# Optimization experiments

Measured on AMD Instinct MI355X. Metric: run time of the kernel, lower is better.

## Reference

```python
import jax, jax.numpy as jnp
import numpy as np

D_MODEL = 1024
NUM_HEADS = 16
D_HEAD = D_MODEL // NUM_HEADS
THETA = 10000.0
NEG_INF = -1e9


def apply_rope(x, theta=THETA):
    # x: (..., S, Dh) with interleaved pairs (2i, 2i+1)
    S, Dh = x.shape[-2], x.shape[-1]
    inv_freq = 1.0 / (theta ** (jnp.arange(0, Dh, 2, dtype=jnp.float32) / Dh))  # (Dh/2,)
    ang = jnp.arange(S, dtype=jnp.float32)[:, None] * inv_freq[None, :]          # (S, Dh/2)
    cos, sin = jnp.cos(ang), jnp.sin(ang)
    x1 = x[..., 0::2]
    x2 = x[..., 1::2]
    r1 = x1 * cos - x2 * sin
    r2 = x1 * sin + x2 * cos
    # interleave back
    return jnp.stack([r1, r2], axis=-1).reshape(x.shape)


def setup_inputs() -> dict:
    key = jax.random.key(0)
    ks = jax.random.split(key, 5)
    B, S = 2, 2048
    scale = 1.0 / np.sqrt(D_MODEL)
    return {
        "x": jax.random.normal(ks[0], (B, S, D_MODEL), dtype=jnp.float32),
        "Wq": jax.random.normal(ks[1], (D_MODEL, D_MODEL), dtype=jnp.float32) * scale,
        "Wk": jax.random.normal(ks[2], (D_MODEL, D_MODEL), dtype=jnp.float32) * scale,
        "Wv": jax.random.normal(ks[3], (D_MODEL, D_MODEL), dtype=jnp.float32) * scale,
        "Wo": jax.random.normal(ks[4], (D_MODEL, D_MODEL), dtype=jnp.float32) * scale,
    }


def reference(x, Wq, Wk, Wv, Wo):
    B, S, _ = x.shape
    def split_heads(t):
        return t.reshape(B, S, NUM_HEADS, D_HEAD).transpose(0, 2, 1, 3)  # (B,H,S,Dh)
    # nn.Linear(bias=False): y = x @ W.T
    Q = split_heads(x @ Wq.T)
    K = split_heads(x @ Wk.T)
    V = split_heads(x @ Wv.T)
    Q = apply_rope(Q)
    K = apply_rope(K)
    scale = 1.0 / jnp.sqrt(jnp.asarray(D_HEAD, dtype=x.dtype))
    scores = jnp.einsum("bhqd,bhkd->bhqk", Q, K) * scale  # (B,H,S,S)
    causal = jnp.tril(jnp.ones((S, S), dtype=bool))
    scores = jnp.where(causal, scores, NEG_INF)
    attn = jax.nn.softmax(scores, axis=-1)
    out = jnp.einsum("bhqk,bhkd->bhqd", attn, V)
    out = out.transpose(0, 2, 1, 3).reshape(B, S, D_MODEL)
    return out @ Wo.T
```

## Files before the change

### kernel.cpp

```cpp
#include <hip/hip_runtime.h>
#include <hip/hip_bf16.h>
#include <stdint.h>

typedef __attribute__((ext_vector_type(8))) short bf8;
typedef __attribute__((ext_vector_type(4))) float f4;

#define MFMA16(a, b, c) __builtin_amdgcn_mfma_f32_16x16x32_bf16((a), (b), (c), 0, 0, 0)

static __device__ __forceinline__ short f2b(float f) {
  uint32_t x = __float_as_uint(f);
  x += 0x7fffu + ((x >> 16) & 1u);
  return (short)(x >> 16);
}

static __device__ __forceinline__ uint32_t cvtpk(float lo, float hi) {
  uint32_t r;
  asm("v_cvt_pk_bf16_f32 %0, %1, %2" : "=v"(r) : "v"(lo), "v"(hi));
  return r;
}

static __device__ __forceinline__ void gload16(const short* g, void* l) {
  __builtin_amdgcn_global_load_lds(
      (const __attribute__((address_space(1))) void*)g,
      (__attribute__((address_space(3))) void*)l, 16, 0, 0);
}

__global__ void convert_kernel(const float* __restrict__ x,
                               const float* __restrict__ wq, const float* __restrict__ wk,
                               const float* __restrict__ wv, const float* __restrict__ wo,
                               short* __restrict__ xb, short* __restrict__ Wb,
                               float2* __restrict__ tab) {
  const int bid = blockIdx.x;
  if (bid >= 4096) {
    const int t = (bid - 4096) * 256 + threadIdx.x;
    const int s = t >> 5, i = t & 31;
    const float inv = powf(10000.0f, -(float)i * (1.0f / 32.0f));
    const float ang = (float)s * inv;
    float sv, cv;
    sincosf(ang, &sv, &cv);
    tab[t] = make_float2(cv, sv);
    return;
  }
  const size_t i = ((size_t)bid * 256 + threadIdx.x) * 8;
  const float* __restrict__ src;
  short* __restrict__ dst;
  if (i < 4194304u) {
    src = x + i;
    dst = xb + i;
  } else {
    const size_t j = i - 4194304u;
    const int z = (int)(j >> 20);
    const size_t o = j & 1048575u;
    src = (z == 0 ? wq : z == 1 ? wk : z == 2 ? wv : wo) + o;
    dst = Wb + j;
  }
  const float4 a = *(const float4*)src;
  const float4 b = *(const float4*)(src + 4);
  bf8 v;
  v[0] = f2b(a.x); v[1] = f2b(a.y); v[2] = f2b(a.z); v[3] = f2b(a.w);
  v[4] = f2b(b.x); v[5] = f2b(b.y); v[6] = f2b(b.z); v[7] = f2b(b.w);
  *(bf8*)dst = v;
}

template <int MODE>
__launch_bounds__(256, 2)
__global__ void gemm_kernel(const short* __restrict__ Ab, const short* __restrict__ Wb,
                            short* __restrict__ Qo, short* __restrict__ Ko,
                            short* __restrict__ VTo, float* __restrict__ Fo,
                            const float2* __restrict__ rope) {
  constexpr int K = 1024;
  const int bm = blockIdx.x, bn = blockIdx.y;
  const int z = (MODE == 0) ? blockIdx.z : 3;
  const short* __restrict__ Bb = Wb + ((size_t)z << 20);

  __shared__ short As[128 * 64];
  __shared__ short Bs[128 * 64];

  const int tid = threadIdx.x;
  const int lane = tid & 63;
  const int wave = tid >> 6;
  const int wr = wave >> 1, wc = wave & 1;
  const int lg = lane >> 4, lr = lane & 15;

  f4 acc[4][4];
#pragma unroll
  for (int i = 0; i < 4; i++)
#pragma unroll
    for (int j = 0; j < 4; j++) {
      acc[i][j][0] = 0.f; acc[i][j][1] = 0.f;
      acc[i][j][2] = 0.f; acc[i][j][3] = 0.f;
    }

  const int kc = tid & 7;
  const int srow = tid >> 3;
  const int kcs = (kc ^ (srow & 7)) * 8;
  char* const Asw = (char*)As + wave * 1024;
  char* const Bsw = (char*)Bs + wave * 1024;

  for (int k0 = 0; k0 < K; k0 += 64) {
#pragma unroll
    for (int i = 0; i < 4; i++) {
      const int row = srow + i * 32;
      gload16(Ab + (size_t)(bm * 128 + row) * K + k0 + kcs, Asw + i * 4096);
      gload16(Bb + (size_t)(bn * 128 + row) * K + k0 + kcs, Bsw + i * 4096);
    }
    __syncthreads();
#pragma unroll
    for (int kk = 0; kk < 2; kk++) {
      bf8 af[4], bb[4];
#pragma unroll
      for (int mi = 0; mi < 4; mi++) {
        const int row = wr * 64 + mi * 16 + lr;
        const int lb = (row * 128 + kk * 64 + lg * 16) ^ ((row & 7) << 4);
        af[mi] = *(const bf8*)((const char*)As + lb);
      }
#pragma unroll
      for (int ni = 0; ni < 4; ni++) {
        const int row = wc * 64 + ni * 16 + lr;
        const int lb = (row * 128 + kk * 64 + lg * 16) ^ ((row & 7) << 4);
        bb[ni] = *(const bf8*)((const char*)Bs + lb);
      }
#pragma unroll
      for (int mi = 0; mi < 4; mi++)
#pragma unroll
        for (int ni = 0; ni < 4; ni++)
          acc[mi][ni] = MFMA16(af[mi], bb[ni], acc[mi][ni]);
    }
    __syncthreads();
  }

  if (MODE == 1) {
#pragma unroll
    for (int mi = 0; mi < 4; mi++) {
      const int m0 = bm * 128 + wr * 64 + mi * 16 + lg * 4;
#pragma unroll
      for (int ni = 0; ni < 4; ni++) {
        const int n = bn * 128 + wc * 64 + ni * 16 + lr;
#pragma unroll
        for (int r = 0; r < 4; r++)
          Fo[(size_t)(m0 + r) * 1024 + n] = acc[mi][ni][r];
      }
    }
    return;
  }

  if (z == 2) {
#pragma unroll
    for (int mi = 0; mi < 4; mi++) {
      const int m0 = bm * 128 + wr * 64 + mi * 16 + lg * 4;
      const int b = m0 >> 11, s0 = m0 & 2047;
#pragma unroll
      for (int ni = 0; ni < 4; ni++) {
        const int n = bn * 128 + wc * 64 + ni * 16 + lr;
        ushort4 pk;
        pk.x = (unsigned short)f2b(acc[mi][ni][0]);
        pk.y = (unsigned short)f2b(acc[mi][ni][1]);
        pk.z = (unsigned short)f2b(acc[mi][ni][2]);
        pk.w = (unsigned short)f2b(acc[mi][ni][3]);
        *(ushort4*)(VTo + ((size_t)((b * 16 + (n >> 6)) * 64 + (n & 63))) * 2048 + s0) = pk;
      }
    }
  } else {
    short* __restrict__ Out = (z == 0) ? Qo : Ko;
    const float qscale = (z == 0) ? 0.18033688011112042f : 1.0f;
#pragma unroll
    for (int mi = 0; mi < 4; mi++) {
      const int m0 = bm * 128 + wr * 64 + mi * 16 + lg * 4;
      const int b = m0 >> 11, s0 = m0 & 2047;
#pragma unroll
      for (int ni = 0; ni < 4; ni++) {
        const int n = bn * 128 + wc * 64 + ni * 16 + lr;
        const int h = n >> 6, d = n & 63;
        const float sgn = (d & 1) ? 1.0f : -1.0f;
#pragma unroll
        for (int r = 0; r < 4; r++) {
          const float v = acc[mi][ni][r];
          const float p = __shfl_xor(v, 1);
          const float2 cs = rope[((s0 + r) << 5) + (d >> 1)];
          const float res = (v * cs.x + sgn * p * cs.y) * qscale;
          Out[((size_t)(b * 16 + h) * 2048 + (s0 + r)) * 64 + d] = f2b(res);
        }
      }
    }
  }
}

__launch_bounds__(512, 4)
__global__ void attn_kernel(const short* __restrict__ Qg, const short* __restrict__ Kg,
                            const short* __restrict__ Vg, short* __restrict__ AO) {
  const int S = 2048;
  const int id = blockIdx.x;
  const int xcd = id & 7, slot = id >> 3;
  const int bh = xcd * 4 + (slot & 3);
  const int qb = 15 - (slot >> 2);
  const int tid = threadIdx.x;
  const int lane = tid & 63, wave = tid >> 6;
  const int lg = lane >> 4, lr = lane & 15;
  const short* __restrict__ Qp = Qg + (size_t)bh * S * 64;
  const short* __restrict__ Kp = Kg + (size_t)bh * S * 64;
  const short* __restrict__ Vp = Vg + (size_t)bh * 64 * S;

  __shared__ short KB[2][2][64 * 64];
  __shared__ short VB[2][2][64 * 64];
  __shared__ short PB[8][16 * 64];

  const int srow = tid >> 3;
  const int kcs = ((tid & 7) ^ (srow & 7)) * 8;

  const int qbase = qb * 128 + wave * 16;
  const int nkv = qb + 1;

  bf8 qf[2];
#pragma unroll
  for (int ks = 0; ks < 2; ks++)
    qf[ks] = *(const bf8*)(Qp + (size_t)(qbase + lr) * 64 + ks * 32 + lg * 8);

  f4 o[4];
#pragma unroll
  for (int dt = 0; dt < 4; dt++) {
    o[dt][0] = 0.f; o[dt][1] = 0.f; o[dt][2] = 0.f; o[dt][3] = 0.f;
  }
  float mrun = -1e30f, lsum = 0.f;

  char* const Pw = (char*)&PB[wave][0];
  const int rowoff = lr * 128;
  const int sw = (lr & 7) << 4;

#pragma unroll
  for (int h = 0; h < 2; h++) {
    gload16(Kp + (size_t)(64 * h + srow) * 64 + kcs, (char*)KB[0][h] + wave * 1024);
    gload16(Vp + (size_t)srow * 2048 + 64 * h + kcs, (char*)VB[0][h] + wave * 1024);
  }
  __syncthreads();

  for (int kb = 0; kb < nkv; kb++) {
    const int kvb = kb * 128;
    const int cur = kb & 1;

    if (kb + 1 < nkv) {
      const int nb = kvb + 128;
#pragma unroll
      for (int h = 0; h < 2; h++) {
        gload16(Kp + (size_t)(nb + 64 * h + srow) * 64 + kcs, (char*)KB[cur ^ 1][h] + wave * 1024);
        gload16(Vp + (size_t)srow * 2048 + nb + 64 * h + kcs, (char*)VB[cur ^ 1][h] + wave * 1024);
      }
    }

#pragma unroll
    for (int h = 0; h < 2; h++) {
      const int kvbh = kvb + 64 * h;
      if (kvbh < qbase + 16) {
        const char* Kc = (const char*)KB[cur][h];
        const char* Vc = (const char*)VB[cur][h];

        f4 st[4];
        __builtin_amdgcn_s_setprio(1);
#pragma unroll
        for (int nt = 0; nt < 4; nt++) {
          const int row = nt * 16 + lr;
          const int base = row * 128 + lg * 16;
          const int rsw = (row & 7) << 4;
          const bf8 k0 = *(const bf8*)(Kc + (base ^ rsw));
          const bf8 k1 = *(const bf8*)(Kc + ((base + 64) ^ rsw));
          f4 c;
          c[0] = 0.f; c[1] = 0.f; c[2] = 0.f; c[3] = 0.f;
          c = MFMA16(k0, qf[0], c);
          c = MFMA16(k1, qf[1], c);
          st[nt] = c;
        }
        __builtin_amdgcn_s_setprio(0);

        if ((kvbh + 63) > qbase) {
          const int q = qbase + lr;
#pragma unroll
          for (int nt = 0; nt < 4; nt++)
#pragma unroll
            for (int r = 0; r < 4; r++) {
              const int kv = kvbh + nt * 16 + lg * 4 + r;
              if (kv > q) st[nt][r] = -1e9f;
            }
        }

        float m0 = fmaxf(fmaxf(st[0][0], st[0][1]), fmaxf(st[0][2], st[0][3]));
#pragma unroll
        for (int nt = 1; nt < 4; nt++)
          m0 = fmaxf(m0, fmaxf(fmaxf(st[nt][0], st[nt][1]), fmaxf(st[nt][2], st[nt][3])));

        if (__any(m0 - mrun > 8.0f)) {
          m0 = fmaxf(m0, __shfl_xor(m0, 16));
          m0 = fmaxf(m0, __shfl_xor(m0, 32));
          const float mn = fmaxf(mrun, m0);
          const float corr = __builtin_amdgcn_exp2f(mrun - mn);
          mrun = mn;
          lsum *= corr;
#pragma unroll
          for (int r = 0; r < 4; r++) {
            const float co = __shfl(corr, (lg << 2) + r);
#pragma unroll
            for (int dt = 0; dt < 4; dt++) o[dt][r] *= co;
          }
        }

        asm volatile("" ::: "memory");

#pragma unroll
        for (int nt = 0; nt < 4; nt++) {
          const float p0 = __builtin_amdgcn_exp2f(st[nt][0] - mrun);
          const float p1 = __builtin_amdgcn_exp2f(st[nt][1] - mrun);
          const float p2 = __builtin_amdgcn_exp2f(st[nt][2] - mrun);
          const float p3 = __builtin_amdgcn_exp2f(st[nt][3] - mrun);
          lsum += (p0 + p1) + (p2 + p3);
          *(uint2*)(Pw + ((rowoff + nt * 32 + lg * 8) ^ sw)) =
              make_uint2(cvtpk(p0, p1), cvtpk(p2, p3));
        }

        asm volatile("" ::: "memory");

        bf8 pf[2];
#pragma unroll
        for (int ks = 0; ks < 2; ks++)
          pf[ks] = *(const bf8*)(Pw + ((rowoff + ks * 64 + lg * 16) ^ sw));

        __builtin_amdgcn_s_setprio(1);
#pragma unroll
        for (int dt = 0; dt < 4; dt++) {
          const int row = dt * 16 + lr;
          const int base = row * 128 + lg * 16;
          const int rsw = (row & 7) << 4;
          const bf8 v0 = *(const bf8*)(Vc + (base ^ rsw));
          const bf8 v1 = *(const bf8*)(Vc + ((base + 64) ^ rsw));
          o[dt] = MFMA16(pf[0], v0, o[dt]);
          o[dt] = MFMA16(pf[1], v1, o[dt]);
        }
        __builtin_amdgcn_s_setprio(0);
      }
    }

    __syncthreads();
  }

  float s = lsum;
  s += __shfl_xor(s, 16);
  s += __shfl_xor(s, 32);
  const float inv = 1.0f / s;
  float inv_o[4];
#pragma unroll
  for (int r = 0; r < 4; r++) inv_o[r] = __shfl(inv, (lg << 2) + r);

  const int b = bh >> 4, h = bh & 15;
#pragma unroll
  for (int r = 0; r < 4; r++) {
    const int q = qbase + lg * 4 + r;
#pragma unroll
    for (int dt = 0; dt < 4; dt++) {
      const int d = dt * 16 + lr;
      AO[((size_t)b * 2048 + q) * 1024 + h * 64 + d] = f2b(o[dt][r] * inv_o[r]);
    }
  }
}

extern "C" void kernel_launch(void* const* d_in, const int* in_sizes, int n_in,
                              void* d_out, int out_size, void* d_ws, size_t ws_size,
                              hipStream_t stream) {
  const float* x  = (const float*)d_in[0];
  const float* wq = (const float*)d_in[1];
  const float* wk = (const float*)d_in[2];
  const float* wv = (const float*)d_in[3];
  const float* wo = (const float*)d_in[4];
  float* out = (float*)d_out;

  char* ws = (char*)d_ws;
  short*  Qb  = (short*)(ws);
  short*  Kb  = (short*)(ws + (8ull  << 20));
  short*  VTb = (short*)(ws + (16ull << 20));
  short*  AOb = (short*)(ws + (24ull << 20));
  short*  xb  = AOb;
  short*  Wb  = (short*)(ws + (32ull << 20));
  float2* tab = (float2*)(ws + (40ull << 20));

  convert_kernel<<<4352, 256, 0, stream>>>(x, wq, wk, wv, wo, xb, Wb, tab);
  gemm_kernel<0><<<dim3(32, 8, 3), 256, 0, stream>>>(
      xb, Wb, Qb, Kb, VTb, nullptr, tab);
  attn_kernel<<<512, 512, 0, stream>>>(Qb, Kb, VTb, AOb);
  gemm_kernel<1><<<dim3(32, 8, 1), 256, 0, stream>>>(
      AOb, Wb, nullptr, nullptr, nullptr, out, nullptr);
}
```

Measured before the change: 105.3 us.

## Double-buffer LDS tiles in projection GEMM to overlap loads with MFMA

The GEMM main loop now uses two shared-memory buffers for A and B tiles. It issues the global-to-LDS loads for the next K-slice before computing on the current one, and keeps a single barrier per iteration. This is meant to hide global load latency behind the matrix-core work. LDS use doubles to 64KB per block, which may limit the two-blocks-per-CU occupancy target. The loads are asynchronous and there is no explicit vmcnt wait before the barrier, so correctness depends on the barrier waiting for them.

```diff
diff --git a/kernel.cpp b/kernel.cpp
--- a/kernel.cpp
+++ b/kernel.cpp
@@ -73,8 +73,8 @@
   const int z = (MODE == 0) ? blockIdx.z : 3;
   const short* __restrict__ Bb = Wb + ((size_t)z << 20);
 
-  __shared__ short As[128 * 64];
-  __shared__ short Bs[128 * 64];
+  __shared__ short As[2][128 * 64];
+  __shared__ short Bs[2][128 * 64];
 
   const int tid = threadIdx.x;
   const int lane = tid & 63;
@@ -94,17 +94,27 @@
   const int kc = tid & 7;
   const int srow = tid >> 3;
   const int kcs = (kc ^ (srow & 7)) * 8;
-  char* const Asw = (char*)As + wave * 1024;
-  char* const Bsw = (char*)Bs + wave * 1024;
-
-  for (int k0 = 0; k0 < K; k0 += 64) {
-#pragma unroll
-    for (int i = 0; i < 4; i++) {
-      const int row = srow + i * 32;
-      gload16(Ab + (size_t)(bm * 128 + row) * K + k0 + kcs, Asw + i * 4096);
-      gload16(Bb + (size_t)(bn * 128 + row) * K + k0 + kcs, Bsw + i * 4096);
-    }
-    __syncthreads();
+
+#define GSTAGE(buf, k0_)                                                          \
+  do {                                                                            \
+    char* const Asw_ = (char*)As[buf] + wave * 1024;                              \
+    char* const Bsw_ = (char*)Bs[buf] + wave * 1024;                              \
+    _Pragma("unroll") for (int i_ = 0; i_ < 4; i_++) {                            \
+      const int row_ = srow + i_ * 32;                                            \
+      gload16(Ab + (size_t)(bm * 128 + row_) * K + (k0_) + kcs, Asw_ + i_ * 4096); \
+      gload16(Bb + (size_t)(bn * 128 + row_) * K + (k0_) + kcs, Bsw_ + i_ * 4096); \
+    }                                                                             \
+  } while (0)
+
+  GSTAGE(0, 0);
+  __syncthreads();
+
+  for (int ks = 0; ks < 16; ks++) {
+    const int cur = ks & 1;
+    if (ks + 1 < 16) GSTAGE(cur ^ 1, (ks + 1) * 64);
+
+    const char* Ac = (const char*)As[cur];
+    const char* Bc = (const char*)Bs[cur];
 #pragma unroll
     for (int kk = 0; kk < 2; kk++) {
       bf8 af[4], bb[4];
@@ -112,13 +122,13 @@
       for (int mi = 0; mi < 4; mi++) {
         const int row = wr * 64 + mi * 16 + lr;
         const int lb = (row * 128 + kk * 64 + lg * 16) ^ ((row & 7) << 4);
-        af[mi] = *(const bf8*)((const char*)As + lb);
+        af[mi] = *(const bf8*)(Ac + lb);
       }
 #pragma unroll
       for (int ni = 0; ni < 4; ni++) {
         const int row = wc * 64 + ni * 16 + lr;
         const int lb = (row * 128 + kk * 64 + lg * 16) ^ ((row & 7) << 4);
-        bb[ni] = *(const bf8*)((const char*)Bs + lb);
+        bb[ni] = *(const bf8*)(Bc + lb);
       }
 #pragma unroll
       for (int mi = 0; mi < 4; mi++)
@@ -128,6 +138,7 @@
     }
     __syncthreads();
   }
+#undef GSTAGE
 
   if (MODE == 1) {
 #pragma unroll
```

Result: slower. 110.8 us (+5.3%).
